# Performance work log

Measured on AMD Instinct MI355X. Metric: run time of the kernel, lower is better.

The kernel has to match this reference:

```python
import jax, jax.numpy as jnp
import numpy as np

B, S, D, H = 2, 2048, 768, 12
DH = D // H  # 64


def setup_inputs() -> dict:
    key = jax.random.key(0)
    ks = jax.random.split(key, 8)
    std = 1.0 / np.sqrt(D)
    return {
        "q": jax.random.normal(ks[0], (B, S, D), dtype=jnp.float32),
        "k": jax.random.normal(ks[1], (B, S, D), dtype=jnp.float32),
        "v": jax.random.normal(ks[2], (B, S, D), dtype=jnp.float32),
        "Wq": jax.random.normal(ks[3], (D, D), dtype=jnp.float32) * std,
        "bq": jnp.zeros((D,), dtype=jnp.float32),
        "Wk": jax.random.normal(ks[4], (D, D), dtype=jnp.float32) * std,
        "bk": jnp.zeros((D,), dtype=jnp.float32),
        "Wv": jax.random.normal(ks[5], (D, D), dtype=jnp.float32) * std,
        "bv": jnp.zeros((D,), dtype=jnp.float32),
        "Wo": jax.random.normal(ks[6], (D, D), dtype=jnp.float32) * std,
        "bo": jnp.zeros((D,), dtype=jnp.float32),
    }


def reference(q, k, v, Wq, bq, Wk, bk, Wv, bv, Wo, bo):
    b, s, d = q.shape
    # linear projections then split heads: [b, s, d] -> [b, h, s, dh]
    def split(x):
        return x.reshape(b, s, H, DH).transpose(0, 2, 1, 3)

    qh = split(q @ Wq + bq)
    kh = split(k @ Wk + bk)
    vh = split(v @ Wv + bv)

    scale = 1.0 / jnp.sqrt(jnp.asarray(DH, dtype=q.dtype))
    # full [b, h, s, s] score matrix (faithful to the original unfused op)
    scores = jnp.einsum("bhqd,bhkd->bhqk", qh, kh) * scale
    # look-ahead mask: 1 above the diagonal, added as mask * -1e9
    look_ahead = jnp.triu(jnp.ones((s, s), dtype=scores.dtype), k=1)
    scores = scores + look_ahead * (-1e9)

    attn = jax.nn.softmax(scores, axis=-1)  # dropout is identity at inference
    ctx = jnp.einsum("bhqk,bhkd->bhqd", attn, vh)
    ctx = ctx.transpose(0, 2, 1, 3).reshape(b, s, d)
    return ctx @ Wo + bo
```

## Files before the change

kernel.cpp:

```cpp
#include <hip/hip_runtime.h>
#include <hip/hip_bf16.h>
#include <stdint.h>

#define Bz 2
#define Sz 2048
#define Dz 768
#define Hz 12
#define DHz 64
#define Mz (Bz*Sz)
#define NQT2 64

typedef __attribute__((ext_vector_type(4))) float f32x4;
typedef __attribute__((ext_vector_type(8))) short bf16x8;
typedef unsigned short u16;
typedef __attribute__((ext_vector_type(8))) unsigned short u16x8;

__device__ __forceinline__ u16 f2bf(float f) {
  union { float f; uint32_t u; } c; c.f = f;
  uint32_t u = c.u;
  return (u16)((u + 0x7fffu + ((u >> 16) & 1u)) >> 16);
}

#define GLL16(gsrc, ldst) \
  __builtin_amdgcn_global_load_lds((const __attribute__((address_space(1))) void*)(gsrc), \
                                   (__attribute__((address_space(3))) void*)(ldst), 16, 0, 0)

__device__ __forceinline__ f32x4 mfma16(bf16x8 a, bf16x8 b, f32x4 c) {
  return __builtin_amdgcn_mfma_f32_16x16x32_bf16(a, b, c, 0, 0, 0);
}

__global__ void cvt3_kernel(const float* __restrict__ qa, const float* __restrict__ ka,
                            const float* __restrict__ va,
                            u16* __restrict__ qo, u16* __restrict__ ko, u16* __restrict__ vo,
                            int n8) {
  int i = blockIdx.x * blockDim.x + threadIdx.x;
  if (i >= n8) return;
  int z = blockIdx.y;
  const float* src = (z == 0) ? qa : (z == 1) ? ka : va;
  u16* dst = (z == 0) ? qo : (z == 1) ? ko : vo;
  const float4* s4 = (const float4*)src;
  float4 a = s4[(size_t)i * 2];
  float4 b = s4[(size_t)i * 2 + 1];
  u16x8 o;
  o[0] = f2bf(a.x); o[1] = f2bf(a.y); o[2] = f2bf(a.z); o[3] = f2bf(a.w);
  o[4] = f2bf(b.x); o[5] = f2bf(b.y); o[6] = f2bf(b.z); o[7] = f2bf(b.w);
  *(u16x8*)(dst + (size_t)i * 8) = o;
}

__global__ void wtrans4_kernel(const float* __restrict__ W0, const float* __restrict__ W1,
                               const float* __restrict__ W2, const float* __restrict__ W3,
                               u16* __restrict__ T0, u16* __restrict__ T1,
                               u16* __restrict__ T2, u16* __restrict__ T3) {
  __shared__ float tile[32][33];
  int z = blockIdx.z;
  const float* W = (z == 0) ? W0 : (z == 1) ? W1 : (z == 2) ? W2 : W3;
  u16* Wt = (z == 0) ? T0 : (z == 1) ? T1 : (z == 2) ? T2 : T3;
  int bx = blockIdx.x * 32, by = blockIdx.y * 32;
  int tx = threadIdx.x & 31, ty = threadIdx.x >> 5;
#pragma unroll
  for (int i = 0; i < 32; i += 8)
    tile[ty + i][tx] = W[(size_t)(by + ty + i) * Dz + bx + tx];
  __syncthreads();
#pragma unroll
  for (int i = 0; i < 32; i += 8)
    Wt[(size_t)(bx + ty + i) * Dz + by + tx] = f2bf(tile[tx][ty + i]);
}

__device__ __forceinline__ void gemm_core(
    const u16* __restrict__ A, const u16* __restrict__ Wt,
    const float* __restrict__ bias, void* __restrict__ out, int mode, float oscale,
    u16 (*As)[128 * 32], u16 (*Bs)[128 * 32])
{
  const int tid = threadIdx.x;
  const int wid = tid >> 6, lane = tid & 63;
  const int wm = wid >> 1, wn = wid & 1;
  const int m0 = blockIdx.x * 128, n0 = blockIdx.y * 128;
  const int fq = lane >> 4, fr = lane & 15;

  int aoff[2];
#pragma unroll
  for (int c = 0; c < 2; ++c) {
    int off  = (wid * 2 + c) * 1024 + lane * 16;
    int row  = off >> 6;
    int colb = (off & 63) ^ (((row >> 1) & 3) << 4);
    aoff[c]  = row * Dz + (colb >> 1);
  }

  int raddr[4], rbaddr[4];
#pragma unroll
  for (int f = 0; f < 4; ++f) {
    int rowA = wm * 64 + f * 16 + fr;
    raddr[f]  = rowA * 64 + ((fq * 16) ^ (((rowA >> 1) & 3) << 4));
    int rowB = wn * 64 + f * 16 + fr;
    rbaddr[f] = rowB * 64 + ((fq * 16) ^ (((rowB >> 1) & 3) << 4));
  }

  f32x4 acc[4][4];
  const f32x4 zero = {0.f, 0.f, 0.f, 0.f};
#pragma unroll
  for (int i = 0; i < 4; ++i)
#pragma unroll
    for (int j = 0; j < 4; ++j) acc[i][j] = zero;

  const u16* Abase = A + (size_t)m0 * Dz;
  const u16* Bbase = Wt + (size_t)n0 * Dz;

  const int NKT = Dz / 32;
#pragma unroll
  for (int c = 0; c < 2; ++c) {
    GLL16(Abase + aoff[c], (char*)As[0] + (wid * 2 + c) * 1024);
    GLL16(Bbase + aoff[c], (char*)Bs[0] + (wid * 2 + c) * 1024);
  }
  int cur = 0;

  for (int kt = 0; kt < NKT; ++kt) {
    int nx = cur + 1; if (nx == 3) nx = 0;
    if (kt + 1 < NKT) {
      int ke = (kt + 1) * 32;
#pragma unroll
      for (int c = 0; c < 2; ++c) {
        GLL16(Abase + ke + aoff[c], (char*)As[nx] + (wid * 2 + c) * 1024);
        GLL16(Bbase + ke + aoff[c], (char*)Bs[nx] + (wid * 2 + c) * 1024);
      }
      asm volatile("s_waitcnt vmcnt(4)" ::: "memory");
    } else {
      asm volatile("s_waitcnt vmcnt(0)" ::: "memory");
    }
    __builtin_amdgcn_s_barrier();
    __builtin_amdgcn_sched_barrier(0);

    bf16x8 af[4], bf[4];
#pragma unroll
    for (int f = 0; f < 4; ++f) {
      af[f] = *(const bf16x8*)((const char*)As[cur] + raddr[f]);
      bf[f] = *(const bf16x8*)((const char*)Bs[cur] + rbaddr[f]);
    }
    __builtin_amdgcn_s_setprio(1);
#pragma unroll
    for (int i = 0; i < 4; ++i)
#pragma unroll
      for (int j = 0; j < 4; ++j)
        acc[i][j] = mfma16(af[i], bf[j], acc[i][j]);
    __builtin_amdgcn_s_setprio(0);
    cur = nx;
  }

  if (mode == 2) {
    float* O = (float*)out;
#pragma unroll
    for (int i = 0; i < 4; ++i) {
      int grow = m0 + wm * 64 + i * 16 + fq * 4;
#pragma unroll
      for (int j = 0; j < 4; ++j) {
        int gcol = n0 + wn * 64 + j * 16 + fr;
        float bv = bias[gcol];
#pragma unroll
        for (int r = 0; r < 4; ++r)
          O[(size_t)(grow + r) * Dz + gcol] = acc[i][j][r] + bv;
      }
    }
  } else {
    u16* O = (u16*)out;
#pragma unroll
    for (int i = 0; i < 4; ++i) {
      int grow = m0 + wm * 64 + i * 16 + fq * 4;
#pragma unroll
      for (int j = 0; j < 4; ++j) {
        int gcol = n0 + wn * 64 + j * 16 + fr;
        float bv = bias[gcol];
        int h = gcol >> 6, dh = gcol & 63;
#pragma unroll
        for (int r = 0; r < 4; ++r) {
          int t = grow + r;
          int b = t >> 11, s = t & 2047;
          float v = (acc[i][j][r] + bv) * oscale;
          if (mode == 0)
            O[((size_t)(b * Hz + h) * Sz + s) * DHz + dh] = f2bf(v);
          else
            O[((size_t)(b * Hz + h) * DHz + dh) * Sz + s] = f2bf(v);
        }
      }
    }
  }
}

#define QSCALE 0.1803368801111404f

__global__ __launch_bounds__(256, 2) void gemm_qkv(
    const u16* __restrict__ qb, const u16* __restrict__ kb, const u16* __restrict__ vb,
    const u16* __restrict__ Wqt, const u16* __restrict__ Wkt, const u16* __restrict__ Wvt,
    const float* __restrict__ bq, const float* __restrict__ bk, const float* __restrict__ bv,
    u16* __restrict__ Qh, u16* __restrict__ Kh, u16* __restrict__ Vt)
{
  __shared__ u16 As[3][128 * 32];
  __shared__ u16 Bs[3][128 * 32];
  const u16* A; const u16* W; const float* bias; u16* out; int mode; float osc;
  if (blockIdx.z == 0)      { A = qb; W = Wqt; bias = bq; out = Qh; mode = 0; osc = QSCALE; }
  else if (blockIdx.z == 1) { A = kb; W = Wkt; bias = bk; out = Kh; mode = 0; osc = 1.f; }
  else                      { A = vb; W = Wvt; bias = bv; out = Vt; mode = 1; osc = 1.f; }
  gemm_core(A, W, bias, out, mode, osc, As, Bs);
}

__global__ __launch_bounds__(256, 2) void gemm_out_k(
    const u16* __restrict__ ctx, const u16* __restrict__ Wot,
    const float* __restrict__ bo, float* __restrict__ out)
{
  __shared__ u16 As[3][128 * 32];
  __shared__ u16 Bs[3][128 * 32];
  gemm_core(ctx, Wot, bo, (void*)out, 2, 1.f, As, Bs);
}

__device__ __forceinline__ void stage_kv(const u16* __restrict__ Kg, const u16* __restrict__ Vg,
                                         int kt, u16* Ks, u16* Vs, int wid, int lane) {
#pragma unroll
  for (int c = 0; c < 4; ++c) {
    int off  = (wid * 4 + c) * 1024 + lane * 16;
    int row  = off >> 7;
    int colb = (off & 127) ^ ((row & 7) << 4);
    GLL16(Kg + ((size_t)(kt * 64 + row)) * DHz + (colb >> 1), (char*)Ks + (wid * 4 + c) * 1024);
    GLL16(Vg + (size_t)row * Sz + kt * 64 + (colb >> 1),      (char*)Vs + (wid * 4 + c) * 1024);
  }
}

__device__ __forceinline__ void attn_group(
    const bf16x8* aq, const bf16x8 kfr[4][2], const bf16x8 vfr[4][2],
    f32x4* o, float* m_r, float* l_r, char* Pw,
    int qbase, int kt, bool diag, int fq, int fr)
{
  const f32x4 zero = {0.f, 0.f, 0.f, 0.f};
  f32x4 s[4];
#pragma unroll
  for (int j = 0; j < 4; ++j) s[j] = zero;
  __builtin_amdgcn_s_setprio(1);
#pragma unroll
  for (int j = 0; j < 4; ++j)
#pragma unroll
    for (int kk = 0; kk < 2; ++kk)
      s[j] = mfma16(aq[kk], kfr[j][kk], s[j]);
  __builtin_amdgcn_s_setprio(0);

  if (diag) {
#pragma unroll
    for (int j = 0; j < 4; ++j) {
      int keyg = kt * 64 + j * 16 + fr;
#pragma unroll
      for (int r = 0; r < 4; ++r)
        if (keyg > qbase + fq * 4 + r) s[j][r] = -1e30f;
    }
  }

  float mt[4];
#pragma unroll
  for (int r = 0; r < 4; ++r) mt[r] = s[0][r];
#pragma unroll
  for (int j = 1; j < 4; ++j)
#pragma unroll
    for (int r = 0; r < 4; ++r) mt[r] = fmaxf(mt[r], s[j][r]);

  int nd = 0;
#pragma unroll
  for (int r = 0; r < 4; ++r) nd |= (mt[r] > m_r[r] + 8.f) ? 1 : 0;
  if (__any(nd)) {
#pragma unroll
    for (int msk = 1; msk < 16; msk <<= 1)
#pragma unroll
      for (int r = 0; r < 4; ++r) mt[r] = fmaxf(mt[r], __shfl_xor(mt[r], msk));
#pragma unroll
    for (int r = 0; r < 4; ++r) {
      float mn = fmaxf(m_r[r], mt[r]);
      float alpha = __builtin_amdgcn_exp2f(m_r[r] - mn);
      m_r[r] = mn;
      l_r[r] *= alpha;
#pragma unroll
      for (int i = 0; i < 4; ++i) o[i][r] *= alpha;
    }
  }

#pragma unroll
  for (int j = 0; j < 4; ++j) {
#pragma unroll
    for (int r = 0; r < 4; ++r) {
      float e = __builtin_amdgcn_exp2f(s[j][r] - m_r[r]);
      l_r[r] += e;
      int qr = fq * 4 + r;
      int key2 = (j * 16 + fr) * 2;
      *(u16*)(Pw + qr * 128 + (key2 ^ ((qr & 7) << 4))) = f2bf(e);
    }
  }

  __builtin_amdgcn_s_setprio(1);
#pragma unroll
  for (int kk = 0; kk < 2; ++kk) {
    int cbP = (kk * 64 + fq * 16) ^ ((fr & 7) << 4);
    bf16x8 pa = *(const bf16x8*)(Pw + fr * 128 + cbP);
#pragma unroll
    for (int fo = 0; fo < 4; ++fo)
      o[fo] = mfma16(pa, vfr[fo][kk], o[fo]);
  }
  __builtin_amdgcn_s_setprio(0);
}

__global__ __launch_bounds__(128, 2) void attn_kernel(
    const u16* __restrict__ Qh, const u16* __restrict__ Kh,
    const u16* __restrict__ Vt, u16* __restrict__ ctx)
{
  __shared__ u16 Ks[3][64 * 64];
  __shared__ u16 Vs[3][64 * 64];
  __shared__ u16 Ps[2 * 16 * 64];
  const int tid = threadIdx.x, wid = tid >> 6, lane = tid & 63;
  const int fq = lane >> 4, fr = lane & 15;
  const int bh = blockIdx.x;
  const int p = blockIdx.y;
  const int b = bh / Hz, h = bh % Hz;
  const int qb0 = p * 32 + wid * 16;
  const int qb1 = (NQT2 - 1 - p) * 32 + wid * 16;
  const int nkt = ((NQT2 - p) * 32 + 63) / 64;
  const int nlo = ((p + 1) * 32 + 63) / 64;

  const u16* Kg = Kh + (size_t)bh * Sz * DHz;
  const u16* Vg = Vt + (size_t)bh * DHz * Sz;
  const u16* Qg = Qh + (size_t)bh * Sz * DHz;

  bf16x8 aq[2][2];
#pragma unroll
  for (int kk = 0; kk < 2; ++kk) {
    aq[0][kk] = *(const bf16x8*)(Qg + (qb0 + fr) * DHz + kk * 32 + fq * 8);
    aq[1][kk] = *(const bf16x8*)(Qg + (qb1 + fr) * DHz + kk * 32 + fq * 8);
  }

  const f32x4 zero = {0.f, 0.f, 0.f, 0.f};
  f32x4 o[2][4];
#pragma unroll
  for (int g = 0; g < 2; ++g)
#pragma unroll
    for (int i = 0; i < 4; ++i) o[g][i] = zero;
  float m_r[2][4], l_r[2][4];
#pragma unroll
  for (int g = 0; g < 2; ++g)
#pragma unroll
    for (int r = 0; r < 4; ++r) { m_r[g][r] = -1e30f; l_r[g][r] = 0.f; }

  char* Pw = (char*)(Ps + wid * 16 * 64);

  stage_kv(Kg, Vg, 0, Ks[0], Vs[0], wid, lane);
  int cur = 0;

  for (int kt = 0; kt < nkt; ++kt) {
    int nx = cur + 1; if (nx == 3) nx = 0;
    if (kt + 1 < nkt) {
      stage_kv(Kg, Vg, kt + 1, Ks[nx], Vs[nx], wid, lane);
      asm volatile("s_waitcnt vmcnt(8)" ::: "memory");
    } else {
      asm volatile("s_waitcnt vmcnt(0)" ::: "memory");
    }
    __builtin_amdgcn_s_barrier();
    __builtin_amdgcn_sched_barrier(0);

    const char* Kb = (const char*)Ks[cur];
    const char* Vb = (const char*)Vs[cur];

    bf16x8 kfr[4][2];
#pragma unroll
    for (int j = 0; j < 4; ++j) {
      int rowK = j * 16 + fr;
#pragma unroll
      for (int kk = 0; kk < 2; ++kk)
        kfr[j][kk] = *(const bf16x8*)(Kb + rowK * 128 + ((kk * 64 + fq * 16) ^ ((rowK & 7) << 4)));
    }
    bf16x8 vfr[4][2];
#pragma unroll
    for (int fo = 0; fo < 4; ++fo) {
      int rowV = fo * 16 + fr;
#pragma unroll
      for (int kk = 0; kk < 2; ++kk)
        vfr[fo][kk] = *(const bf16x8*)(Vb + rowV * 128 + ((kk * 64 + fq * 16) ^ ((rowV & 7) << 4)));
    }

    if (kt < nlo)
      attn_group(aq[0], kfr, vfr, o[0], m_r[0], l_r[0], Pw, qb0, kt, kt == nlo - 1, fq, fr);
    attn_group(aq[1], kfr, vfr, o[1], m_r[1], l_r[1], Pw, qb1, kt, kt == nkt - 1, fq, fr);

    cur = nx;
  }

#pragma unroll
  for (int msk = 1; msk < 16; msk <<= 1)
#pragma unroll
    for (int g = 0; g < 2; ++g)
#pragma unroll
      for (int r = 0; r < 4; ++r) l_r[g][r] += __shfl_xor(l_r[g][r], msk);

#pragma unroll
  for (int g = 0; g < 2; ++g) {
    int qb = (g == 0) ? qb0 : qb1;
#pragma unroll
    for (int fo = 0; fo < 4; ++fo) {
      int dh = fo * 16 + fr;
#pragma unroll
      for (int r = 0; r < 4; ++r) {
        int qg = qb + fq * 4 + r;
        ctx[((size_t)b * Sz + qg) * Dz + h * DHz + dh] = f2bf(o[g][fo][r] / l_r[g][r]);
      }
    }
  }
}

extern "C" void kernel_launch(void* const* d_in, const int* in_sizes, int n_in,
                              void* d_out, int out_size, void* d_ws, size_t ws_size,
                              hipStream_t stream) {
  const float* q  = (const float*)d_in[0];
  const float* k  = (const float*)d_in[1];
  const float* v  = (const float*)d_in[2];
  const float* Wq = (const float*)d_in[3];
  const float* bq = (const float*)d_in[4];
  const float* Wk = (const float*)d_in[5];
  const float* bk = (const float*)d_in[6];
  const float* Wv = (const float*)d_in[7];
  const float* bv = (const float*)d_in[8];
  const float* Wo = (const float*)d_in[9];
  const float* bo = (const float*)d_in[10];
  float* out = (float*)d_out;

  char* ws = (char*)d_ws;
  size_t off = 0;
  auto alloc = [&](size_t bytes) {
    void* p = ws + off;
    off += (bytes + 255) & ~(size_t)255;
    return p;
  };
  u16* qb  = (u16*)alloc((size_t)Mz * Dz * 2);
  u16* kb  = (u16*)alloc((size_t)Mz * Dz * 2);
  u16* vb  = (u16*)alloc((size_t)Mz * Dz * 2);
  u16* Wqt = (u16*)alloc((size_t)Dz * Dz * 2);
  u16* Wkt = (u16*)alloc((size_t)Dz * Dz * 2);
  u16* Wvt = (u16*)alloc((size_t)Dz * Dz * 2);
  u16* Wot = (u16*)alloc((size_t)Dz * Dz * 2);
  u16* Qh  = (u16*)alloc((size_t)Bz * Hz * Sz * DHz * 2);
  u16* Kh  = (u16*)alloc((size_t)Bz * Hz * Sz * DHz * 2);
  u16* Vtr = (u16*)alloc((size_t)Bz * Hz * DHz * Sz * 2);
  u16* ctx = (u16*)alloc((size_t)Mz * Dz * 2);

  int n8 = Mz * Dz / 8;
  int cblk = (n8 + 255) / 256;
  cvt3_kernel<<<dim3(cblk, 3), 256, 0, stream>>>(q, k, v, qb, kb, vb, n8);

  wtrans4_kernel<<<dim3(Dz / 32, Dz / 32, 4), 256, 0, stream>>>(
      Wq, Wk, Wv, Wo, Wqt, Wkt, Wvt, Wot);

  gemm_qkv<<<dim3(Mz / 128, Dz / 128, 3), 256, 0, stream>>>(
      qb, kb, vb, Wqt, Wkt, Wvt, bq, bk, bv, Qh, Kh, Vtr);

  attn_kernel<<<dim3(Bz * Hz, NQT2 / 2), 128, 0, stream>>>(Qh, Kh, Vtr, ctx);

  gemm_out_k<<<dim3(Mz / 128, Dz / 128), 256, 0, stream>>>(ctx, Wot, bo, out);
}
```

Before: 104.3 us.

## Write Q/K/V in MFMA fragment order and load attention operands directly to registers

The QKV projection epilogue now scatters its outputs into a fragment-major layout, so each lane's bf16x8 MFMA operand sits contiguously. The attention kernel drops LDS staging, the triple buffer and the per-tile barriers for K/V, and loads K (prefetched one tile ahead) and V straight from global memory into registers. This removes LDS traffic and block-wide synchronisation. In exchange, each wave now fetches K/V independently instead of sharing them through LDS, which raises global/L2 traffic and exposes V load latency. The epilogue stores also become more scattered.

```diff
diff --git a/kernel.cpp b/kernel.cpp
--- a/kernel.cpp
+++ b/kernel.cpp
@@ -173,11 +173,20 @@
         for (int r = 0; r < 4; ++r) {
           int t = grow + r;
           int b = t >> 11, s = t & 2047;
-          float v = (acc[i][j][r] + bv) * oscale;
-          if (mode == 0)
-            O[((size_t)(b * Hz + h) * Sz + s) * DHz + dh] = f2bf(v);
-          else
-            O[((size_t)(b * Hz + h) * DHz + dh) * Sz + s] = f2bf(v);
+          int bh = b * Hz + h;
+          u16 val = f2bf((acc[i][j][r] + bv) * oscale);
+          size_t idx;
+          if (mode == 0) {
+            idx = ((((size_t)bh * 128 + (s >> 4)) * 2 + (dh >> 5)) * 64
+                   + ((dh >> 3) & 3) * 16 + (s & 15)) * 8 + (dh & 7);
+          } else if (mode == 3) {
+            idx = (((((size_t)bh * 32 + (s >> 6)) * 4 + ((s >> 4) & 3)) * 2 + (dh >> 5)) * 64
+                   + ((dh >> 3) & 3) * 16 + (s & 15)) * 8 + (dh & 7);
+          } else {
+            idx = (((((size_t)bh * 32 + (s >> 6)) * 4 + (dh >> 4)) * 2 + ((s >> 5) & 1)) * 64
+                   + ((s >> 3) & 3) * 16 + (dh & 15)) * 8 + (s & 7);
+          }
+          O[idx] = val;
         }
       }
     }
@@ -190,14 +199,14 @@
     const u16* __restrict__ qb, const u16* __restrict__ kb, const u16* __restrict__ vb,
     const u16* __restrict__ Wqt, const u16* __restrict__ Wkt, const u16* __restrict__ Wvt,
     const float* __restrict__ bq, const float* __restrict__ bk, const float* __restrict__ bv,
-    u16* __restrict__ Qh, u16* __restrict__ Kh, u16* __restrict__ Vt)
+    u16* __restrict__ Qf, u16* __restrict__ Kf, u16* __restrict__ Vf)
 {
   __shared__ u16 As[3][128 * 32];
   __shared__ u16 Bs[3][128 * 32];
   const u16* A; const u16* W; const float* bias; u16* out; int mode; float osc;
-  if (blockIdx.z == 0)      { A = qb; W = Wqt; bias = bq; out = Qh; mode = 0; osc = QSCALE; }
-  else if (blockIdx.z == 1) { A = kb; W = Wkt; bias = bk; out = Kh; mode = 0; osc = 1.f; }
-  else                      { A = vb; W = Wvt; bias = bv; out = Vt; mode = 1; osc = 1.f; }
+  if (blockIdx.z == 0)      { A = qb; W = Wqt; bias = bq; out = Qf; mode = 0; osc = QSCALE; }
+  else if (blockIdx.z == 1) { A = kb; W = Wkt; bias = bk; out = Kf; mode = 3; osc = 1.f; }
+  else                      { A = vb; W = Wvt; bias = bv; out = Vf; mode = 1; osc = 1.f; }
   gemm_core(A, W, bias, out, mode, osc, As, Bs);
 }
 
@@ -210,18 +219,6 @@
   gemm_core(ctx, Wot, bo, (void*)out, 2, 1.f, As, Bs);
 }
 
-__device__ __forceinline__ void stage_kv(const u16* __restrict__ Kg, const u16* __restrict__ Vg,
-                                         int kt, u16* Ks, u16* Vs, int wid, int lane) {
-#pragma unroll
-  for (int c = 0; c < 4; ++c) {
-    int off  = (wid * 4 + c) * 1024 + lane * 16;
-    int row  = off >> 7;
-    int colb = (off & 127) ^ ((row & 7) << 4);
-    GLL16(Kg + ((size_t)(kt * 64 + row)) * DHz + (colb >> 1), (char*)Ks + (wid * 4 + c) * 1024);
-    GLL16(Vg + (size_t)row * Sz + kt * 64 + (colb >> 1),      (char*)Vs + (wid * 4 + c) * 1024);
-  }
-}
-
 __device__ __forceinline__ void attn_group(
     const bf16x8* aq, const bf16x8 kfr[4][2], const bf16x8 vfr[4][2],
     f32x4* o, float* m_r, float* l_r, char* Pw,
@@ -301,11 +298,9 @@
 }
 
 __global__ __launch_bounds__(128, 2) void attn_kernel(
-    const u16* __restrict__ Qh, const u16* __restrict__ Kh,
-    const u16* __restrict__ Vt, u16* __restrict__ ctx)
+    const u16* __restrict__ Qf, const u16* __restrict__ Kf,
+    const u16* __restrict__ Vf, u16* __restrict__ ctx)
 {
-  __shared__ u16 Ks[3][64 * 64];
-  __shared__ u16 Vs[3][64 * 64];
   __shared__ u16 Ps[2 * 16 * 64];
   const int tid = threadIdx.x, wid = tid >> 6, lane = tid & 63;
   const int fq = lane >> 4, fr = lane & 15;
@@ -317,15 +312,15 @@
   const int nkt = ((NQT2 - p) * 32 + 63) / 64;
   const int nlo = ((p + 1) * 32 + 63) / 64;
 
-  const u16* Kg = Kh + (size_t)bh * Sz * DHz;
-  const u16* Vg = Vt + (size_t)bh * DHz * Sz;
-  const u16* Qg = Qh + (size_t)bh * Sz * DHz;
+  const bf16x8* Qf8 = (const bf16x8*)Qf + (size_t)bh * 128 * 2 * 64;
+  const bf16x8* Kf8 = (const bf16x8*)Kf + (size_t)bh * 32 * 8 * 64;
+  const bf16x8* Vf8 = (const bf16x8*)Vf + (size_t)bh * 32 * 8 * 64;
 
   bf16x8 aq[2][2];
 #pragma unroll
   for (int kk = 0; kk < 2; ++kk) {
-    aq[0][kk] = *(const bf16x8*)(Qg + (qb0 + fr) * DHz + kk * 32 + fq * 8);
-    aq[1][kk] = *(const bf16x8*)(Qg + (qb1 + fr) * DHz + kk * 32 + fq * 8);
+    aq[0][kk] = Qf8[((size_t)(qb0 >> 4) * 2 + kk) * 64 + lane];
+    aq[1][kk] = Qf8[((size_t)(qb1 >> 4) * 2 + kk) * 64 + lane];
   }
 
   const f32x4 zero = {0.f, 0.f, 0.f, 0.f};
@@ -342,45 +337,38 @@
 
   char* Pw = (char*)(Ps + wid * 16 * 64);
 
-  stage_kv(Kg, Vg, 0, Ks[0], Vs[0], wid, lane);
-  int cur = 0;
+  bf16x8 kfr[4][2], knx[4][2], vfr[4][2];
+#pragma unroll
+  for (int j = 0; j < 4; ++j)
+#pragma unroll
+    for (int kk = 0; kk < 2; ++kk)
+      kfr[j][kk] = Kf8[(size_t)(j * 2 + kk) * 64 + lane];
 
   for (int kt = 0; kt < nkt; ++kt) {
-    int nx = cur + 1; if (nx == 3) nx = 0;
+#pragma unroll
+    for (int fo = 0; fo < 4; ++fo)
+#pragma unroll
+      for (int kk = 0; kk < 2; ++kk)
+        vfr[fo][kk] = Vf8[((size_t)kt * 8 + fo * 2 + kk) * 64 + lane];
     if (kt + 1 < nkt) {
-      stage_kv(Kg, Vg, kt + 1, Ks[nx], Vs[nx], wid, lane);
-      asm volatile("s_waitcnt vmcnt(8)" ::: "memory");
-    } else {
-      asm volatile("s_waitcnt vmcnt(0)" ::: "memory");
-    }
-    __builtin_amdgcn_s_barrier();
-    __builtin_amdgcn_sched_barrier(0);
-
-    const char* Kb = (const char*)Ks[cur];
-    const char* Vb = (const char*)Vs[cur];
-
-    bf16x8 kfr[4][2];
-#pragma unroll
-    for (int j = 0; j < 4; ++j) {
-      int rowK = j * 16 + fr;
-#pragma unroll
-      for (int kk = 0; kk < 2; ++kk)
-        kfr[j][kk] = *(const bf16x8*)(Kb + rowK * 128 + ((kk * 64 + fq * 16) ^ ((rowK & 7) << 4)));
-    }
-    bf16x8 vfr[4][2];
-#pragma unroll
-    for (int fo = 0; fo < 4; ++fo) {
-      int rowV = fo * 16 + fr;
-#pragma unroll
-      for (int kk = 0; kk < 2; ++kk)
-        vfr[fo][kk] = *(const bf16x8*)(Vb + rowV * 128 + ((kk * 64 + fq * 16) ^ ((rowV & 7) << 4)));
+#pragma unroll
+      for (int j = 0; j < 4; ++j)
+#pragma unroll
+        for (int kk = 0; kk < 2; ++kk)
+          knx[j][kk] = Kf8[((size_t)(kt + 1) * 8 + j * 2 + kk) * 64 + lane];
     }
 
     if (kt < nlo)
       attn_group(aq[0], kfr, vfr, o[0], m_r[0], l_r[0], Pw, qb0, kt, kt == nlo - 1, fq, fr);
     attn_group(aq[1], kfr, vfr, o[1], m_r[1], l_r[1], Pw, qb1, kt, kt == nkt - 1, fq, fr);
 
-    cur = nx;
+    if (kt + 1 < nkt) {
+#pragma unroll
+      for (int j = 0; j < 4; ++j)
+#pragma unroll
+        for (int kk = 0; kk < 2; ++kk)
+          kfr[j][kk] = knx[j][kk];
+    }
   }
 
 #pragma unroll
@@ -435,9 +423,9 @@
   u16* Wkt = (u16*)alloc((size_t)Dz * Dz * 2);
   u16* Wvt = (u16*)alloc((size_t)Dz * Dz * 2);
   u16* Wot = (u16*)alloc((size_t)Dz * Dz * 2);
-  u16* Qh  = (u16*)alloc((size_t)Bz * Hz * Sz * DHz * 2);
-  u16* Kh  = (u16*)alloc((size_t)Bz * Hz * Sz * DHz * 2);
-  u16* Vtr = (u16*)alloc((size_t)Bz * Hz * DHz * Sz * 2);
+  u16* Qf  = (u16*)alloc((size_t)Bz * Hz * Sz * DHz * 2);
+  u16* Kf  = (u16*)alloc((size_t)Bz * Hz * Sz * DHz * 2);
+  u16* Vf  = (u16*)alloc((size_t)Bz * Hz * Sz * DHz * 2);
   u16* ctx = (u16*)alloc((size_t)Mz * Dz * 2);
 
   int n8 = Mz * Dz / 8;
@@ -448,9 +436,9 @@
       Wq, Wk, Wv, Wo, Wqt, Wkt, Wvt, Wot);
 
   gemm_qkv<<<dim3(Mz / 128, Dz / 128, 3), 256, 0, stream>>>(
-      qb, kb, vb, Wqt, Wkt, Wvt, bq, bk, bv, Qh, Kh, Vtr);
-
-  attn_kernel<<<dim3(Bz * Hz, NQT2 / 2), 128, 0, stream>>>(Qh, Kh, Vtr, ctx);
+      qb, kb, vb, Wqt, Wkt, Wvt, bq, bk, bv, Qf, Kf, Vf);
+
+  attn_kernel<<<dim3(Bz * Hz, NQT2 / 2), 128, 0, stream>>>(Qf, Kf, Vf, ctx);
 
   gemm_out_k<<<dim3(Mz / 128, Dz / 128), 256, 0, stream>>>(ctx, Wot, bo, out);
 }
```

Measured after the change: 98.11 us. -5.9%, faster.
